# Performance work log

Hardware: AMD Instinct MI355X
Metric: run time of the kernel (lower is better)

Reference implementation:

```python
import jax, jax.numpy as jnp
from jax import lax
import numpy as np

T_NO = 50       # history / kernel half-length (hard-coded in module)
T_MAX = 101     # basis kernel length = 2*T_NO + 1
BASIS_NO = 34
HIST_BASIS_NO = 18
SIGMA = 3.0
HID = 20
SUB = 20


def _make_basis(n_basis, length):
    # basis[i, t] = exp(-(t - 3*i)^2 / sigma)
    raw = jnp.arange(length, dtype=jnp.float32)
    pts = 3.0 * jnp.arange(n_basis, dtype=jnp.float32)
    return jnp.exp(-((raw[None, :] - pts[:, None]) ** 2) / SIGMA)


def _conv1d(x, kern, pad):
    # x: [1, Cin, T], kern: [Cout, Cin, K] -> [1, Cout, T'] (torch F.conv1d semantics, cross-correlation)
    return lax.conv_general_dilated(x, kern, window_strides=(1,), padding=[(pad, pad)],
                                    dimension_numbers=('NCH', 'OIH', 'NCH'))


def setup_inputs() -> dict:
    key = jax.random.key(0)
    ks = jax.random.split(key, 12)
    T, Ee, Ei = 200000, 500, 100
    S_e = (jax.random.uniform(ks[0], (T, Ee)) < 0.05).astype(jnp.float32)
    S_i = (jax.random.uniform(ks[1], (T, Ei)) < 0.05).astype(jnp.float32)
    # one-hot synapse->subunit connectivity, as in the original model
    C_syn_e = jax.nn.one_hot(jax.random.randint(ks[2], (Ee,), 0, SUB), SUB, dtype=jnp.float32).T
    C_syn_i = jax.nn.one_hot(jax.random.randint(ks[3], (Ei,), 0, SUB), SUB, dtype=jnp.float32).T
    weight1 = 0.01 * jax.random.normal(ks[4], (HID, 2 * SUB, BASIS_NO), dtype=jnp.float32)
    weight4 = 0.01 * jax.random.normal(ks[5], (1, HID, BASIS_NO), dtype=jnp.float32)
    W_hist = 0.01 * jax.random.normal(ks[6], (HIST_BASIS_NO,), dtype=jnp.float32)
    Theta = 0.01 * jax.random.normal(ks[7], (1,), dtype=jnp.float32)
    W_spk = jnp.ones((1,), jnp.float32)
    Tau_spk = 3.0 * jnp.ones((1,), jnp.float32)
    u = jax.random.uniform(ks[8], (T,), dtype=jnp.float32)  # bernoulli noise
    return dict(S_e=S_e, S_i=S_i, C_syn_e=C_syn_e, C_syn_i=C_syn_i,
                weight1=weight1, weight4=weight4, W_hist=W_hist, Theta=Theta,
                W_spk=W_spk, Tau_spk=Tau_spk, u=u)


def reference(S_e, S_i, C_syn_e, C_syn_i, weight1, weight4, W_hist, Theta, W_spk, Tau_spk, u):
    basis = _make_basis(BASIS_NO, T_MAX)          # [34, 101]
    hist_basis = _make_basis(HIST_BASIS_NO, T_NO)  # [18, 50]

    kern1 = jnp.einsum('hsb,bt->hst', weight1, basis)  # [HID, 2*SUB, 101]
    kern4 = jnp.einsum('ohb,bt->oht', weight4, basis)  # [1, HID, 101]

    # route synapses to subunits, stack e/i: [1, 2*SUB, T]
    syn_in = jnp.concatenate([S_e @ C_syn_e.T, S_i @ C_syn_i.T], axis=1).T[None]
    out1 = jax.nn.leaky_relu(_conv1d(syn_in, kern1, T_NO), 0.01)  # [1, HID, T]
    out4 = _conv1d(out1, kern4, T_NO)[0, 0]                        # [T]

    hist_kern = W_hist @ hist_basis  # [50]
    theta = Theta[0]

    def step(buf, inp):
        # buf: last T_NO spikes, oldest first (== spk_out[t:t+T_NO])
        o_t, u_t = inp
        p = jax.nn.sigmoid(o_t + buf @ hist_kern + theta)
        spk = (u_t < p).astype(jnp.float32)  # torch.bernoulli(p)
        buf = jnp.concatenate([buf[1:], spk[None]])
        return buf, (p, spk)

    buf0 = jnp.zeros((T_NO,), jnp.float32)
    _, (prob_out, spikes) = lax.scan(step, buf0, (out4, u))
    spk_out = jnp.concatenate([jnp.zeros((T_NO,), jnp.float32), spikes])  # [T + T_NO]

    t = jnp.arange(T_NO, dtype=jnp.float32)
    t_tau = t / (Tau_spk[0] ** 2)
    spk_kern = t_tau * jnp.exp(-t_tau) * (W_spk[0] ** 2)  # unflipped; torch flips then cross-correlates
    # torch conv1d(x, flip(k), valid) == jnp.convolve(x, k, 'valid')
    spk_filt = jnp.convolve(spk_out, spk_kern, mode='valid')[:-1]  # [T]
    return (spk_filt, prob_out)
```

## Files before the change

kernel.cpp:

```cpp
#include <hip/hip_runtime.h>
#include <math.h>

#define T_TOT  200000
#define EE     500
#define EI     100
#define SUBN   20
#define NCH    40
#define HIDN   20
#define BNO    34
#define TM     101
#define TNO    50
#define HBNO   18
#define TT1    256
#define EPSF   2e-5f
#define NTAP   58
#define CPT    12

#define PADL   64
#define PADR   256
#define SROW   (PADL + T_TOT + PADR)

#define GROW   (T_TOT + 112)

#define GW     355
#define SW     380
#define CW     (2 * NTAP * CPT)

#define RTILE  512
#define RHALO  64
#define RRND   4
#define NT2    ((T_TOT + RTILE - 1) / RTILE)

__global__ void k_setup(const float* __restrict__ Ce, const float* __restrict__ Ci,
                        const float* __restrict__ Wh, const float* __restrict__ Wspk,
                        const float* __restrict__ Tau,
                        int* __restrict__ ae, int* __restrict__ ai,
                        float* __restrict__ hkpos, float* __restrict__ hkneg,
                        float* __restrict__ spkk, float* __restrict__ gtap,
                        double* __restrict__ hkd, double* __restrict__ basisd)
{
    int tid = threadIdx.x;
    if (tid < EE) {
        int a = 0;
        for (int s = 0; s < SUBN; ++s) if (Ce[s * EE + tid] > 0.5f) a = s;
        ae[tid] = a;
    } else if (tid < EE + EI) {
        int e = tid - EE; int a = 0;
        for (int s = 0; s < SUBN; ++s) if (Ci[s * EI + e] > 0.5f) a = s;
        ai[e] = a;
    } else if (tid < 664) {
        int j = tid - 600;
        double hk = 0.0;
        if (j >= 1 && j <= TNO) {
            int i = TNO - j;
            for (int b = 0; b < HBNO; ++b) {
                double d = (double)i - 3.0 * (double)b;
                hk += (double)Wh[b] * exp(-d * d / 3.0);
            }
        }
        hkd[j] = hk;
        hkpos[j] = (float)fmax(hk, 0.0);
        hkneg[j] = (float)fmin(hk, 0.0);
    } else if (tid < 728) {
        int m = tid - 664; float v = 0.f;
        if (m < TNO) {
            double tau2 = (double)Tau[0] * (double)Tau[0];
            double tt = (double)m / tau2;
            v = (float)(tt * exp(-tt) * (double)Wspk[0] * (double)Wspk[0]);
        }
        spkk[m] = v;
    } else if (tid < 753) {
        int j = tid - 740;
        gtap[tid - 728] = (float)exp(-(double)(j * j) / 3.0);
    }
    for (int idx = tid; idx < BNO * TM; idx += blockDim.x) {
        int b = idx / TM, k = idx % TM;
        double d = (double)k - 3.0 * (double)b;
        basisd[idx] = exp(-d * d / 3.0);
    }
}

__global__ void k_prep(const float* __restrict__ w1, const float* __restrict__ w4,
                       const double* __restrict__ basisd,
                       float* __restrict__ kern4, float* __restrict__ cmerged,
                       float* __restrict__ syn)
{
    int idx = blockIdx.x * 256 + threadIdx.x;
    if (idx < HIDN * TM) {
        int h = idx % HIDN, k = idx / HIDN;
        double acc = 0.0;
        for (int b = 0; b < BNO; ++b) acc += (double)w4[h * BNO + b] * basisd[b * TM + k];
        kern4[k * HIDN + h] = (float)acc;
    } else if (idx < 2020 + NCH * CW) {
        int j = idx - 2020;
        int f = j % CPT, tap = (j / CPT) % NTAP, hg = (j / (CPT * NTAP)) & 1, s = j / CW;
        float val = 0.f;
        if (f < 10) {
            int h = hg * 10 + f;
            if (tap < BNO) {
                val = w1[(h * NCH + s) * BNO + tap];
            } else {
                int mi = tap - BNO;
                int m = (mi < 12) ? (mi - 62) : (mi + 39);
                double acc = 0.0;
                for (int b = 0; b < BNO; ++b) {
                    int jj = m + 50 - 3 * b;
                    if (jj >= -12 && jj <= 12)
                        acc += (double)w1[(h * NCH + s) * BNO + b] * exp(-(double)(jj * jj) / 3.0);
                }
                val = -(float)acc;
            }
        }
        cmerged[j] = val;
    } else if (idx < 2020 + NCH * CW + NCH * (PADL + PADR)) {
        int j = idx - (2020 + NCH * CW);
        int r = j / (PADL + PADR), c = j % (PADL + PADR);
        int off = (c < PADL) ? c : (PADL + T_TOT + (c - PADL));
        syn[(size_t)r * SROW + off] = 0.f;
    }
}

__global__ __launch_bounds__(256) void k_route(const float* __restrict__ Se,
                                               const float* __restrict__ Si,
                                               const int* __restrict__ ae,
                                               const int* __restrict__ ai,
                                               float* __restrict__ syn)
{
    __shared__ float acc[NCH * 64];
    __shared__ int sae[EE];
    __shared__ int sai[EI];
    int tid = threadIdx.x;
    for (int i = tid; i < NCH * 64; i += 256) acc[i] = 0.f;
    for (int i = tid; i < EE; i += 256) sae[i] = ae[i];
    for (int i = tid; i < EI; i += 256) sai[i] = ai[i];
    __syncthreads();
    int t0 = blockIdx.x * 64;
    int lane = tid & 63, grp = tid >> 6;
    for (int ec = 0; ec < 2; ++ec) {
        int ev = ec * 64 + lane;
        if (ev < EE / 4) {
            int e = 4 * ev;
            int a0 = sae[e], a1 = sae[e + 1], a2 = sae[e + 2], a3 = sae[e + 3];
            for (int ts = grp; ts < 64; ts += 8) {
                float4 v1 = *(const float4*)(Se + (size_t)(t0 + ts) * EE + e);
                float4 v2 = *(const float4*)(Se + (size_t)(t0 + ts + 4) * EE + e);
                if (v1.x != 0.f) atomicAdd(&acc[a0 * 64 + ts], v1.x);
                if (v1.y != 0.f) atomicAdd(&acc[a1 * 64 + ts], v1.y);
                if (v1.z != 0.f) atomicAdd(&acc[a2 * 64 + ts], v1.z);
                if (v1.w != 0.f) atomicAdd(&acc[a3 * 64 + ts], v1.w);
                if (v2.x != 0.f) atomicAdd(&acc[a0 * 64 + ts + 4], v2.x);
                if (v2.y != 0.f) atomicAdd(&acc[a1 * 64 + ts + 4], v2.y);
                if (v2.z != 0.f) atomicAdd(&acc[a2 * 64 + ts + 4], v2.z);
                if (v2.w != 0.f) atomicAdd(&acc[a3 * 64 + ts + 4], v2.w);
            }
        }
    }
    {
        int ev = lane;
        if (ev < EI / 4) {
            int e = 4 * ev;
            int a0 = sai[e] + SUBN, a1 = sai[e + 1] + SUBN, a2 = sai[e + 2] + SUBN, a3 = sai[e + 3] + SUBN;
            for (int ts = grp; ts < 64; ts += 8) {
                float4 v1 = *(const float4*)(Si + (size_t)(t0 + ts) * EI + e);
                float4 v2 = *(const float4*)(Si + (size_t)(t0 + ts + 4) * EI + e);
                if (v1.x != 0.f) atomicAdd(&acc[a0 * 64 + ts], v1.x);
                if (v1.y != 0.f) atomicAdd(&acc[a1 * 64 + ts], v1.y);
                if (v1.z != 0.f) atomicAdd(&acc[a2 * 64 + ts], v1.z);
                if (v1.w != 0.f) atomicAdd(&acc[a3 * 64 + ts], v1.w);
                if (v2.x != 0.f) atomicAdd(&acc[a0 * 64 + ts + 4], v2.x);
                if (v2.y != 0.f) atomicAdd(&acc[a1 * 64 + ts + 4], v2.y);
                if (v2.z != 0.f) atomicAdd(&acc[a2 * 64 + ts + 4], v2.z);
                if (v2.w != 0.f) atomicAdd(&acc[a3 * 64 + ts + 4], v2.w);
            }
        }
    }
    __syncthreads();
    for (int i = tid; i < NCH * 64; i += 256) {
        int s = i >> 6, ts = i & 63;
        syn[(size_t)s * SROW + PADL + t0 + ts] = acc[i];
    }
}

__global__ __launch_bounds__(256) void k_prefilt(const float* __restrict__ syn,
                                                 const float* __restrict__ gtap,
                                                 float* __restrict__ G)
{
    int gi = blockIdx.x * 256 + threadIdx.x;
    if (gi >= GROW) return;
    const float* sp = syn + (size_t)blockIdx.y * SROW + PADL + (gi - 50);
    double a = 0.0;
#pragma unroll
    for (int j = -12; j <= 12; ++j)
        a += (double)gtap[j + 12] * (double)sp[j];
    G[(size_t)blockIdx.y * GROW + gi] = (float)a;
}

#define FMA10(c0, c1, c2, v0, v1)                                              \
    acc[0][0] = fmaf(c0.x, v0, acc[0][0]); acc[0][1] = fmaf(c0.x, v1, acc[0][1]); \
    acc[1][0] = fmaf(c0.y, v0, acc[1][0]); acc[1][1] = fmaf(c0.y, v1, acc[1][1]); \
    acc[2][0] = fmaf(c0.z, v0, acc[2][0]); acc[2][1] = fmaf(c0.z, v1, acc[2][1]); \
    acc[3][0] = fmaf(c0.w, v0, acc[3][0]); acc[3][1] = fmaf(c0.w, v1, acc[3][1]); \
    acc[4][0] = fmaf(c1.x, v0, acc[4][0]); acc[4][1] = fmaf(c1.x, v1, acc[4][1]); \
    acc[5][0] = fmaf(c1.y, v0, acc[5][0]); acc[5][1] = fmaf(c1.y, v1, acc[5][1]); \
    acc[6][0] = fmaf(c1.z, v0, acc[6][0]); acc[6][1] = fmaf(c1.z, v1, acc[6][1]); \
    acc[7][0] = fmaf(c1.w, v0, acc[7][0]); acc[7][1] = fmaf(c1.w, v1, acc[7][1]); \
    acc[8][0] = fmaf(c2.x, v0, acc[8][0]); acc[8][1] = fmaf(c2.x, v1, acc[8][1]); \
    acc[9][0] = fmaf(c2.y, v0, acc[9][0]); acc[9][1] = fmaf(c2.y, v1, acc[9][1]);

__global__ __launch_bounds__(256) void k_conv1w(const float* __restrict__ G,
                                                const float* __restrict__ syn,
                                                const float* __restrict__ cmerged,
                                                float* __restrict__ out1)
{
    __shared__ float sg[2][GW];
    __shared__ float ss[2][SW];
    int tid = threadIdx.x;
    int wv = tid >> 6, lane = tid & 63;
    int hg = __builtin_amdgcn_readfirstlane(wv & 1);
    int tsub = wv >> 1;
    int tloc = tsub * 128 + lane;
    int t0 = blockIdx.x * 256;

    {
        const float* Gp = G + t0;
        const float* sp = syn + PADL + t0 - 62;
        for (int i = tid; i < GW; i += 256) sg[0][i] = (t0 + i < GROW) ? Gp[i] : 0.f;
        for (int i = tid; i < SW; i += 256) ss[0][i] = sp[i];
    }

    float acc[10][2];
#pragma unroll
    for (int hh = 0; hh < 10; ++hh) { acc[hh][0] = 0.f; acc[hh][1] = 0.f; }

    for (int s = 0; s < NCH; ++s) {
        __syncthreads();
        int cb = s & 1, nb = cb ^ 1;
        if (s + 1 < NCH) {
            const float* Gp = G + (size_t)(s + 1) * GROW + t0;
            const float* sp = syn + (size_t)(s + 1) * SROW + PADL + t0 - 62;
            for (int i = tid; i < GW; i += 256) sg[nb][i] = (t0 + i < GROW) ? Gp[i] : 0.f;
            for (int i = tid; i < SW; i += 256) ss[nb][i] = sp[i];
        }
        const float* sgc = sg[cb] + tloc;
        const float* ssc = ss[cb] + tloc;
        const float* cc = cmerged + (size_t)s * CW + hg * (NTAP * CPT);
#pragma unroll 4
        for (int b = 0; b < BNO; ++b) {
            float v0 = sgc[3 * b], v1 = sgc[3 * b + 64];
            const float* cp = cc + b * CPT;
            float4 c0 = *(const float4*)cp;
            float4 c1 = *(const float4*)(cp + 4);
            float2 c2 = *(const float2*)(cp + 8);
            FMA10(c0, c1, c2, v0, v1)
        }
#pragma unroll 4
        for (int mi = 0; mi < 12; ++mi) {
            float v0 = ssc[mi], v1 = ssc[mi + 64];
            const float* cp = cc + (BNO + mi) * CPT;
            float4 c0 = *(const float4*)cp;
            float4 c1 = *(const float4*)(cp + 4);
            float2 c2 = *(const float2*)(cp + 8);
            FMA10(c0, c1, c2, v0, v1)
        }
#pragma unroll 4
        for (int mi = 12; mi < 24; ++mi) {
            float v0 = ssc[mi + 101], v1 = ssc[mi + 165];
            const float* cp = cc + (BNO + mi) * CPT;
            float4 c0 = *(const float4*)cp;
            float4 c1 = *(const float4*)(cp + 4);
            float2 c2 = *(const float2*)(cp + 8);
            FMA10(c0, c1, c2, v0, v1)
        }
    }
    int t1 = t0 + tloc, t2 = t1 + 64;
#pragma unroll
    for (int hh = 0; hh < 10; ++hh) {
        int h = hg * 10 + hh;
        float o0 = acc[hh][0], o1 = acc[hh][1];
        if (t1 < T_TOT) out1[(size_t)h * T_TOT + t1] = (o0 > 0.f) ? o0 : 0.01f * o0;
        if (t2 < T_TOT) out1[(size_t)h * T_TOT + t2] = (o1 > 0.f) ? o1 : 0.01f * o1;
    }
}

__global__ __launch_bounds__(256) void k_conv2(const float* __restrict__ out1,
                                               const float* __restrict__ kern4,
                                               const float* __restrict__ Theta,
                                               const float* __restrict__ u,
                                               double* __restrict__ xd,
                                               double* __restrict__ thrd,
                                               float* __restrict__ thr32,
                                               float* __restrict__ blo,
                                               float* __restrict__ bhi)
{
    __shared__ float s1[HIDN * (TT1 + 100)];
    int tid = threadIdx.x;
    int t0 = blockIdx.x * TT1;
    for (int i = tid; i < HIDN * (TT1 + 100); i += 256) {
        int h = i / (TT1 + 100), x = i % (TT1 + 100);
        int g = t0 + x - TNO;
        s1[i] = (g >= 0 && g < T_TOT) ? out1[(size_t)h * T_TOT + g] : 0.f;
    }
    __syncthreads();
    int t = t0 + tid;
    if (t >= T_TOT) return;
    double acc = 0.0;
    for (int k = 0; k < TM; ++k) {
        const float* kp = kern4 + k * HIDN;
#pragma unroll
        for (int h = 0; h < HIDN; ++h)
            acc = fma((double)s1[h * (TT1 + 100) + tid + k], (double)kp[h], acc);
    }
    double x = acc + (double)Theta[0];
    double uu = (double)u[t];
    double th = (log(uu) - log1p(-uu)) - x;
    xd[t] = x; thrd[t] = th; thr32[t] = (float)th;
    blo[t + TNO] = 0.f;
    bhi[t + TNO] = 1.f;
    if (t < TNO) { blo[t] = 0.f; bhi[t] = 0.f; }
    if (t < 14)  { blo[T_TOT + TNO + t] = 0.f; bhi[T_TOT + TNO + t] = 0.f; }
}

__global__ __launch_bounds__(256) void k_relax(const float* __restrict__ thr32,
                                               const float* __restrict__ hkpos,
                                               const float* __restrict__ hkneg,
                                               float* __restrict__ blo,
                                               float* __restrict__ bhi,
                                               int wd, int* __restrict__ dirty)
{
    __shared__ float slo[RTILE + RHALO], shi[RTILE + RHALO];
    __shared__ float sth[RTILE + RHALO];
    __shared__ float shp[64], shn[64];
    int tid = threadIdx.x;
    int t0 = blockIdx.x * RTILE;
    for (int i = tid; i < RTILE + RHALO; i += 256) {
        int t = t0 - RHALO + i;
        int g = t + TNO;
        bool ok = (g >= 0 && g < T_TOT + 64);
        slo[i] = ok ? blo[g] : 0.f;
        shi[i] = ok ? bhi[g] : 0.f;
        sth[i] = (t >= 0 && t < T_TOT) ? thr32[t] : 0.f;
    }
    if (tid < 64) { shp[tid] = hkpos[tid]; shn[tid] = hkneg[tid]; }
    __syncthreads();
    for (int r = 0; r < RRND; ++r) {
        for (int i = tid; i < RTILE + RHALO; i += 256) {
            if (i < TNO) continue;
            float l = slo[i], h = shi[i];
            if (l == h) continue;
            float lo = 0.f, hi = 0.f;
            for (int j = 1; j <= TNO; ++j) {
                float bl = slo[i - j], bh = shi[i - j];
                float hp = shp[j], hn = shn[j];
                lo = fmaf(hp, bl, lo); lo = fmaf(hn, bh, lo);
                hi = fmaf(hp, bh, hi); hi = fmaf(hn, bl, hi);
            }
            float th = sth[i];
            if (lo > th + EPSF)      slo[i] = 1.f;
            else if (hi < th - EPSF) shi[i] = 0.f;
        }
        __syncthreads();
    }
    for (int i = tid; i < RTILE; i += 256) {
        int t = t0 + i;
        if (t < T_TOT) {
            blo[t + TNO] = slo[RHALO + i];
            bhi[t + TNO] = shi[RHALO + i];
        }
    }
    if (wd) {
        int i1 = tid, i2 = tid + 256;
        int u1 = (t0 + i1 < T_TOT) && (slo[RHALO + i1] != shi[RHALO + i1]);
        int u2 = (t0 + i2 < T_TOT) && (slo[RHALO + i2] != shi[RHALO + i2]);
        int c = __syncthreads_count(u1);
        c += __syncthreads_count(u2);
        if (tid == 0) dirty[blockIdx.x] = c;
    }
}

__global__ __launch_bounds__(512) void k_compact(const float* __restrict__ blo,
                                                 const float* __restrict__ bhi,
                                                 const int* __restrict__ dirty,
                                                 const double* __restrict__ hkd,
                                                 int* __restrict__ list,
                                                 int* __restrict__ utot,
                                                 double* __restrict__ afix)
{
    __shared__ int wsum[8];
    __shared__ int sd[NT2];
    __shared__ int sbase;
    int tid = threadIdx.x;
    for (int i = tid; i < NT2; i += 512) sd[i] = dirty[i];
    int t = blockIdx.x * 512 + tid;
    int unk = (t < T_TOT) && (blo[t + TNO] != bhi[t + TNO]);
    unsigned long long m = __ballot(unk);
    int lane = tid & 63, wv = tid >> 6;
    int lr = __popcll(m & ((1ull << lane) - 1ull));
    if (lane == 0) wsum[wv] = __popcll(m);
    __syncthreads();
    if (tid == 0) {
        int b = 0;
        for (int k = 0; k < (int)blockIdx.x; ++k) b += sd[k];
        sbase = b;
        if (blockIdx.x == 0) {
            int tot = 0;
            for (int k = 0; k < NT2; ++k) tot += sd[k];
            utot[0] = tot;
        }
        int r = 0;
        for (int k = 0; k < 8; ++k) { int c = wsum[k]; wsum[k] = r; r += c; }
    }
    __syncthreads();
    if (unk) {
        int pos = sbase + wsum[wv] + lr;
        list[pos] = t;
        double a = 0.0;
        for (int j = 1; j <= TNO; ++j)
            a += hkd[j] * (double)blo[t - j + TNO];
        afix[pos] = a;
    }
}

__global__ __launch_bounds__(1024) void k_chainres(const int* __restrict__ list,
                                                   const double* __restrict__ afix,
                                                   const double* __restrict__ thrd,
                                                   const double* __restrict__ hkd,
                                                   const int* __restrict__ utot,
                                                   int* __restrict__ chead,
                                                   int* __restrict__ bits,
                                                   float* __restrict__ blo,
                                                   float* __restrict__ bhi)
{
    __shared__ double shk[64];
    __shared__ int wcnt[16];
    __shared__ int base_s;
    int tid = threadIdx.x, lane = tid & 63, wv = tid >> 6;
    if (tid < 64) shk[tid] = (tid >= 1 && tid <= TNO) ? hkd[tid] : 0.0;
    if (tid == 0) base_s = 0;
    int U = utot[0];
    __syncthreads();
    for (int b0 = 0; b0 < U; b0 += 1024) {
        int i = b0 + tid;
        int head = 0;
        if (i < U) head = (i == 0) || (list[i] - list[i - 1] > TNO);
        unsigned long long m = __ballot(head);
        int pre = __popcll(m & ((1ull << lane) - 1ull));
        if (lane == 0) wcnt[wv] = __popcll(m);
        __syncthreads();
        int wbase = 0;
        for (int k = 0; k < wv; ++k) wbase += wcnt[k];
        int tot = 0;
        for (int k = 0; k < 16; ++k) tot += wcnt[k];
        if (head) chead[base_s + wbase + pre] = i;
        __syncthreads();
        if (tid == 0) base_s += tot;
        __syncthreads();
    }
    int nch = base_s;
    for (int c = tid; c < nch; c += 1024) {
        int i0 = chead[c];
        int i1 = (c + 1 < nch) ? chead[c + 1] : U;
        for (int i = i0; i < i1; ++i) {
            int t = list[i];
            double a = afix[i];
            for (int k = i - 1; k >= i0; --k) {
                int dt = t - list[k];
                if (dt > TNO) break;
                if (bits[k]) a += shk[dt];
            }
            int sb = (a > thrd[t]) ? 1 : 0;
            bits[i] = sb;
            float f = (float)sb;
            blo[t + TNO] = f;
            bhi[t + TNO] = f;
        }
    }
}

__global__ __launch_bounds__(256) void k_out(const float* __restrict__ blo,
                                             const float* __restrict__ spkk,
                                             const double* __restrict__ hkd,
                                             const double* __restrict__ xd,
                                             float* __restrict__ outp)
{
    __shared__ float sb[TT1 + 64];
    __shared__ float ssp[64];
    __shared__ double shk[64];
    int tid = threadIdx.x;
    int t0 = blockIdx.x * TT1;
    for (int i = tid; i < TT1 + TNO; i += 256) {
        int g = t0 + i;
        sb[i] = (g < T_TOT + 64) ? blo[g] : 0.f;
    }
    if (tid < 64) { ssp[tid] = spkk[tid]; shk[tid] = hkd[tid]; }
    __syncthreads();
    int t = t0 + tid;
    if (t >= T_TOT) return;
    float filt = 0.f;
    double a = 0.0;
    for (int m = 1; m <= TNO; ++m) {
        float b = sb[tid + TNO - m];
        filt = fmaf(b, ssp[m - 1], filt);
        a += shk[m] * (double)b;
    }
    double p = 1.0 / (1.0 + exp(-(xd[t] + a)));
    outp[t] = filt;
    outp[T_TOT + t] = (float)p;
}

extern "C" void kernel_launch(void* const* d_in, const int* in_sizes, int n_in,
                              void* d_out, int out_size, void* d_ws, size_t ws_size,
                              hipStream_t stream)
{
    (void)in_sizes; (void)n_in; (void)out_size; (void)ws_size;
    const float* Se = (const float*)d_in[0];
    const float* Si = (const float*)d_in[1];
    const float* Ce = (const float*)d_in[2];
    const float* Ci = (const float*)d_in[3];
    const float* w1 = (const float*)d_in[4];
    const float* w4 = (const float*)d_in[5];
    const float* Wh = (const float*)d_in[6];
    const float* Th = (const float*)d_in[7];
    const float* Ws = (const float*)d_in[8];
    const float* Ta = (const float*)d_in[9];
    const float* u  = (const float*)d_in[10];

    char* w = (char*)d_ws;
    size_t off = 0;
    auto alloc = [&](size_t n) { size_t o = off; off += (n + 15) & ~(size_t)15; return o; };

    size_t gzone = alloc((size_t)NCH * GROW * 4);
    float*  G     = (float*)(w + gzone);
    double* xd    = (double*)(w + gzone);
    double* thrd  = (double*)(w + gzone + 1600000);
    float*  thr32 = (float*)(w + gzone + 3200000);
    float*  blo   = (float*)(w + gzone + 4000000);
    float*  bhi   = (float*)(w + gzone + 4800512);
    int*    dirty = (int*)(w + gzone + 5601024);
    int*    utot  = (int*)(w + gzone + 5603072);
    int*    list  = (int*)(w + gzone + 5603200);
    double* afix  = (double*)(w + gzone + 6403200);
    int*    chead = (int*)(w + gzone + 8003200);
    int*    bits  = (int*)(w + gzone + 8803216);

    float*  syn     = (float*)(w + alloc((size_t)NCH * SROW * 4));
    float*  out1    = (float*)(w + alloc((size_t)HIDN * T_TOT * 4));
    float*  kern4   = (float*)(w + alloc((size_t)TM * HIDN * 4));
    float*  cmerged = (float*)(w + alloc((size_t)NCH * CW * 4));
    double* basisd  = (double*)(w + alloc((size_t)BNO * TM * 8));
    int*    ae      = (int*)(w + alloc(EE * 4));
    int*    ai      = (int*)(w + alloc(EI * 4));
    float*  hkpos   = (float*)(w + alloc(64 * 4));
    float*  hkneg   = (float*)(w + alloc(64 * 4));
    float*  spkk    = (float*)(w + alloc(64 * 4));
    float*  gtap    = (float*)(w + alloc(32 * 4));
    double* hkd     = (double*)(w + alloc(64 * 8));

    k_setup<<<1, 1024, 0, stream>>>(Ce, Ci, Wh, Ws, Ta, ae, ai, hkpos, hkneg, spkk, gtap, hkd, basisd);
    int prepN = 2020 + NCH * CW + NCH * (PADL + PADR);
    k_prep<<<(prepN + 255) / 256, 256, 0, stream>>>(w1, w4, basisd, kern4, cmerged, syn);
    k_route<<<T_TOT / 64, 256, 0, stream>>>(Se, Si, ae, ai, syn);
    dim3 pg((GROW + 255) / 256, NCH);
    k_prefilt<<<pg, 256, 0, stream>>>(syn, gtap, G);
    k_conv1w<<<(T_TOT + 255) / 256, 256, 0, stream>>>(G, syn, cmerged, out1);
    k_conv2<<<(T_TOT + TT1 - 1) / TT1, 256, 0, stream>>>(out1, kern4, Th, u, xd, thrd, thr32, blo, bhi);
    k_relax<<<NT2, 256, 0, stream>>>(thr32, hkpos, hkneg, blo, bhi, 0, dirty);
    k_relax<<<NT2, 256, 0, stream>>>(thr32, hkpos, hkneg, blo, bhi, 1, dirty);
    k_compact<<<NT2, 512, 0, stream>>>(blo, bhi, dirty, hkd, list, utot, afix);
    k_chainres<<<1, 1024, 0, stream>>>(list, afix, thrd, hkd, utot, chead, bits, blo, bhi);
    k_out<<<(T_TOT + TT1 - 1) / TT1, 256, 0, stream>>>(blo, spkk, hkd, xd, (float*)d_out);
}
```

Baseline: 1.213 ms.

## Register-block conv1 over eight time points per thread and stage weights in LDS

Restructures the first conv kernel so each thread computes 8 time points by 10 hidden channels instead of 2 by 10. Blocks shrink to 128 threads covering 512 time steps. Per-channel merged weights are double-buffered into shared memory instead of being read from global memory. This raises FMA-per-load reuse and cuts redundant weight fetches, but it raises register pressure to 80 accumulators, halves the block count and lowers occupancy.

```diff
diff --git a/kernel.cpp b/kernel.cpp
--- a/kernel.cpp
+++ b/kernel.cpp
@@ -22,8 +22,9 @@
 
 #define GROW   (T_TOT + 112)
 
-#define GW     355
-#define SW     380
+#define C1TB   512
+#define GW2    (C1TB + 99)
+#define SW2    (C1TB + 124)
 #define CW     (2 * NTAP * CPT)
 
 #define RTILE  512
@@ -195,42 +196,32 @@
     G[(size_t)blockIdx.y * GROW + gi] = (float)a;
 }
 
-#define FMA10(c0, c1, c2, v0, v1)                                              \
-    acc[0][0] = fmaf(c0.x, v0, acc[0][0]); acc[0][1] = fmaf(c0.x, v1, acc[0][1]); \
-    acc[1][0] = fmaf(c0.y, v0, acc[1][0]); acc[1][1] = fmaf(c0.y, v1, acc[1][1]); \
-    acc[2][0] = fmaf(c0.z, v0, acc[2][0]); acc[2][1] = fmaf(c0.z, v1, acc[2][1]); \
-    acc[3][0] = fmaf(c0.w, v0, acc[3][0]); acc[3][1] = fmaf(c0.w, v1, acc[3][1]); \
-    acc[4][0] = fmaf(c1.x, v0, acc[4][0]); acc[4][1] = fmaf(c1.x, v1, acc[4][1]); \
-    acc[5][0] = fmaf(c1.y, v0, acc[5][0]); acc[5][1] = fmaf(c1.y, v1, acc[5][1]); \
-    acc[6][0] = fmaf(c1.z, v0, acc[6][0]); acc[6][1] = fmaf(c1.z, v1, acc[6][1]); \
-    acc[7][0] = fmaf(c1.w, v0, acc[7][0]); acc[7][1] = fmaf(c1.w, v1, acc[7][1]); \
-    acc[8][0] = fmaf(c2.x, v0, acc[8][0]); acc[8][1] = fmaf(c2.x, v1, acc[8][1]); \
-    acc[9][0] = fmaf(c2.y, v0, acc[9][0]); acc[9][1] = fmaf(c2.y, v1, acc[9][1]);
-
-__global__ __launch_bounds__(256) void k_conv1w(const float* __restrict__ G,
+__global__ __launch_bounds__(128) void k_conv1w(const float* __restrict__ G,
                                                 const float* __restrict__ syn,
                                                 const float* __restrict__ cmerged,
                                                 float* __restrict__ out1)
 {
-    __shared__ float sg[2][GW];
-    __shared__ float ss[2][SW];
-    int tid = threadIdx.x;
-    int wv = tid >> 6, lane = tid & 63;
-    int hg = __builtin_amdgcn_readfirstlane(wv & 1);
-    int tsub = wv >> 1;
-    int tloc = tsub * 128 + lane;
-    int t0 = blockIdx.x * 256;
+    __shared__ __align__(16) float sg[2][GW2];
+    __shared__ __align__(16) float ss[2][SW2];
+    __shared__ __align__(16) float sc[2][CW];
+    int tid = threadIdx.x;
+    int hg = tid >> 6;
+    int lane = tid & 63;
+    int t0 = blockIdx.x * C1TB;
 
     {
         const float* Gp = G + t0;
         const float* sp = syn + PADL + t0 - 62;
-        for (int i = tid; i < GW; i += 256) sg[0][i] = (t0 + i < GROW) ? Gp[i] : 0.f;
-        for (int i = tid; i < SW; i += 256) ss[0][i] = sp[i];
-    }
-
-    float acc[10][2];
-#pragma unroll
-    for (int hh = 0; hh < 10; ++hh) { acc[hh][0] = 0.f; acc[hh][1] = 0.f; }
+        for (int i = tid; i < GW2; i += 128) sg[0][i] = (t0 + i < GROW) ? Gp[i] : 0.f;
+        for (int i = tid; i < SW2; i += 128) ss[0][i] = sp[i];
+        for (int i = tid; i < CW; i += 128) sc[0][i] = cmerged[i];
+    }
+
+    float acc[10][8];
+#pragma unroll
+    for (int hh = 0; hh < 10; ++hh)
+#pragma unroll
+        for (int k = 0; k < 8; ++k) acc[hh][k] = 0.f;
 
     for (int s = 0; s < NCH; ++s) {
         __syncthreads();
@@ -238,47 +229,74 @@
         if (s + 1 < NCH) {
             const float* Gp = G + (size_t)(s + 1) * GROW + t0;
             const float* sp = syn + (size_t)(s + 1) * SROW + PADL + t0 - 62;
-            for (int i = tid; i < GW; i += 256) sg[nb][i] = (t0 + i < GROW) ? Gp[i] : 0.f;
-            for (int i = tid; i < SW; i += 256) ss[nb][i] = sp[i];
-        }
-        const float* sgc = sg[cb] + tloc;
-        const float* ssc = ss[cb] + tloc;
-        const float* cc = cmerged + (size_t)s * CW + hg * (NTAP * CPT);
-#pragma unroll 4
+            const float* cp = cmerged + (size_t)(s + 1) * CW;
+            for (int i = tid; i < GW2; i += 128) sg[nb][i] = (t0 + i < GROW) ? Gp[i] : 0.f;
+            for (int i = tid; i < SW2; i += 128) ss[nb][i] = sp[i];
+            for (int i = tid; i < CW; i += 128) sc[nb][i] = cp[i];
+        }
+        const float* sgc = sg[cb] + lane;
+        const float* ssc = ss[cb] + lane;
+        const float* cc = sc[cb] + hg * (NTAP * CPT);
+#pragma unroll 2
         for (int b = 0; b < BNO; ++b) {
-            float v0 = sgc[3 * b], v1 = sgc[3 * b + 64];
             const float* cp = cc + b * CPT;
             float4 c0 = *(const float4*)cp;
             float4 c1 = *(const float4*)(cp + 4);
             float2 c2 = *(const float2*)(cp + 8);
-            FMA10(c0, c1, c2, v0, v1)
-        }
-#pragma unroll 4
-        for (int mi = 0; mi < 12; ++mi) {
-            float v0 = ssc[mi], v1 = ssc[mi + 64];
+            float v[8];
+#pragma unroll
+            for (int k = 0; k < 8; ++k) v[k] = sgc[3 * b + 64 * k];
+#pragma unroll
+            for (int k = 0; k < 8; ++k) {
+                acc[0][k] = fmaf(c0.x, v[k], acc[0][k]);
+                acc[1][k] = fmaf(c0.y, v[k], acc[1][k]);
+                acc[2][k] = fmaf(c0.z, v[k], acc[2][k]);
+                acc[3][k] = fmaf(c0.w, v[k], acc[3][k]);
+                acc[4][k] = fmaf(c1.x, v[k], acc[4][k]);
+                acc[5][k] = fmaf(c1.y, v[k], acc[5][k]);
+                acc[6][k] = fmaf(c1.z, v[k], acc[6][k]);
+                acc[7][k] = fmaf(c1.w, v[k], acc[7][k]);
+                acc[8][k] = fmaf(c2.x, v[k], acc[8][k]);
+                acc[9][k] = fmaf(c2.y, v[k], acc[9][k]);
+            }
+        }
+#pragma unroll 2
+        for (int mi = 0; mi < 24; ++mi) {
+            int doff = (mi < 12) ? mi : (mi + 101);
             const float* cp = cc + (BNO + mi) * CPT;
             float4 c0 = *(const float4*)cp;
             float4 c1 = *(const float4*)(cp + 4);
             float2 c2 = *(const float2*)(cp + 8);
-            FMA10(c0, c1, c2, v0, v1)
-        }
-#pragma unroll 4
-        for (int mi = 12; mi < 24; ++mi) {
-            float v0 = ssc[mi + 101], v1 = ssc[mi + 165];
-            const float* cp = cc + (BNO + mi) * CPT;
-            float4 c0 = *(const float4*)cp;
-            float4 c1 = *(const float4*)(cp + 4);
-            float2 c2 = *(const float2*)(cp + 8);
-            FMA10(c0, c1, c2, v0, v1)
-        }
-    }
-    int t1 = t0 + tloc, t2 = t1 + 64;
+            float v[8];
+#pragma unroll
+            for (int k = 0; k < 8; ++k) v[k] = ssc[doff + 64 * k];
+#pragma unroll
+            for (int k = 0; k < 8; ++k) {
+                acc[0][k] = fmaf(c0.x, v[k], acc[0][k]);
+                acc[1][k] = fmaf(c0.y, v[k], acc[1][k]);
+                acc[2][k] = fmaf(c0.z, v[k], acc[2][k]);
+                acc[3][k] = fmaf(c0.w, v[k], acc[3][k]);
+                acc[4][k] = fmaf(c1.x, v[k], acc[4][k]);
+                acc[5][k] = fmaf(c1.y, v[k], acc[5][k]);
+                acc[6][k] = fmaf(c1.z, v[k], acc[6][k]);
+                acc[7][k] = fmaf(c1.w, v[k], acc[7][k]);
+                acc[8][k] = fmaf(c2.x, v[k], acc[8][k]);
+                acc[9][k] = fmaf(c2.y, v[k], acc[9][k]);
+            }
+        }
+    }
+    int tb = t0 + lane;
 #pragma unroll
     for (int hh = 0; hh < 10; ++hh) {
         int h = hg * 10 + hh;
-        float o0 = acc[hh][0], o1 = acc[hh][1];
-        if (t1 < T_TOT) out1[(size_t)h * T_TOT + t1] = (o0 > 0.f) ? o0 : 0.01f * o0;
-        if (t2 < T_TOT) out1[(size_t)h * T_TOT + t2] = (o1 > 0.f) ? o1 : 0.01f * o1;
+#pragma unroll
+        for (int k = 0; k < 8; ++k) {
+            int t = tb + 64 * k;
+            if (t < T_TOT) {
+                float o = acc[hh][k];
+                out1[(size_t)h * T_TOT + t] = (o > 0.f) ? o : 0.01f * o;
+            }
+        }
     }
 }
 
@@ -561,7 +579,7 @@
     k_route<<<T_TOT / 64, 256, 0, stream>>>(Se, Si, ae, ai, syn);
     dim3 pg((GROW + 255) / 256, NCH);
     k_prefilt<<<pg, 256, 0, stream>>>(syn, gtap, G);
-    k_conv1w<<<(T_TOT + 255) / 256, 256, 0, stream>>>(G, syn, cmerged, out1);
+    k_conv1w<<<(T_TOT + C1TB - 1) / C1TB, 128, 0, stream>>>(G, syn, cmerged, out1);
     k_conv2<<<(T_TOT + TT1 - 1) / TT1, 256, 0, stream>>>(out1, kern4, Th, u, xd, thrd, thr32, blo, bhi);
     k_relax<<<NT2, 256, 0, stream>>>(thr32, hkpos, hkneg, blo, bhi, 0, dirty);
     k_relax<<<NT2, 256, 0, stream>>>(thr32, hkpos, hkneg, blo, bhi, 1, dirty);
```

New measurement: 1.343 ms. 1.11x slower.
